# Kernel tuning notes

Measured on AMD Instinct MI355X. Metric: run time of the kernel, lower is better.

Reference implementation:

```python
import jax, jax.numpy as jnp
import numpy as np

N, H, D = 500000, 64, 32  # agents, action_decoder_hidden_dim, distance_embedding_dim


def setup_inputs() -> dict:
    key = jax.random.key(0)
    ks = jax.random.split(key, 8)
    return {
        "action_hidden_state": jax.random.normal(ks[0], (N, H), jnp.float32),
        "goal_hidden_state": jax.random.normal(ks[1], (H,), jnp.float32),
        "goal": jax.random.normal(ks[2], (N, 2), jnp.float32),
        "position": jax.random.normal(ks[3], (N, 2), jnp.float32),
        "W_emb": jax.random.normal(ks[4], (D, 2), jnp.float32) * 0.1,
        "b_emb": jax.random.normal(ks[5], (D,), jnp.float32) * 0.1,
        "W_fc": jax.random.normal(ks[6], (H, 2 * D + 2 * H), jnp.float32) * 0.05,
        "b_fc": jax.random.normal(ks[7], (H,), jnp.float32) * 0.05,
        "idx": 0,
    }


def _distances(a1, a2, g1, g2):
    # a1, g1: (2,); a2, g2: (n, 2). Faithful vectorization of cal_distance,
    # including its algebraic quirks (dn first term is 0; cross_g uses g1[0] twice;
    # n2 mixes a1[1]-a2[0]).
    dn = -(a1[1] - a2[:, 1]) * (g1[0] - g2[:, 0])
    cross_a = a1[0] * a2[:, 1] - a1[1] * a2[:, 0]
    cross_g = g1[0] * g2[:, 1] - g1[0] * g2[:, 0]
    n1 = cross_a * (g1[0] - g2[:, 0]) - (a1[0] - a2[:, 0]) * cross_g
    n2 = cross_a * (g1[1] - g2[:, 1]) - (a1[1] - a2[:, 0]) * cross_g
    d1_base = jnp.linalg.norm(a1 - g1)                 # scalar
    d2_base = jnp.linalg.norm(a2 - g2, axis=-1)        # (n,)
    safe_dn = jnp.where(dn != 0, dn, 1.0)
    p1 = n1 / safe_dn
    p2 = n2 / safe_dn
    cond = (dn != 0) & ((a1[0] - p1) * (p1 - g1[0]) > 0)
    d1_int = jnp.sqrt((a1[0] - p1) ** 2 + (a1[1] - p2) ** 2)
    d2_int = jnp.sqrt((a2[:, 0] - p1) ** 2 + (a2[:, 1] - p2) ** 2)
    return jnp.where(cond, d1_int, d1_base), jnp.where(cond, d2_int, d2_base)


def reference(action_hidden_state, goal_hidden_state, goal, position, W_emb, b_emb, W_fc, b_fc, idx):
    h = action_hidden_state                      # (n, H)
    n, Hd = h.shape
    p_idx = position[idx]                        # (2,)
    d1, d2 = _distances(p_idx, goal, p_idx, position)   # (n,), (n,)
    # embedding(d) with scalar d broadcast to [d, d]: d*(W[:,0]+W[:,1]) + b
    w_sum = W_emb[:, 0] + W_emb[:, 1]            # (D,)
    d1e = d1[:, None] * w_sum[None, :] + b_emb   # (n, D)
    d2e = d2[:, None] * w_sum[None, :] + b_emb   # (n, D)
    h_idx_row = jnp.broadcast_to(h[idx], (n, Hd))
    fc_in = jnp.concatenate([h_idx_row, h, d1e, d2e], axis=1)  # (n, 2H+2D)
    new_h = jax.nn.sigmoid(fc_in @ W_fc.T + b_fc)              # (n, H)
    keep = (jnp.arange(n) == idx)[:, None]       # row idx is skipped in the loop
    h_out = jnp.where(keep, h, new_h)
    # goal update (uses original h[idx], unchanged by the loop)
    dg = jnp.linalg.norm(p_idx - goal[idx])
    dge = dg * w_sum + b_emb                     # (D,)
    fc_in_g = jnp.concatenate([h[idx], goal_hidden_state, dge, dge], axis=0)
    goal_out = jax.nn.sigmoid(W_fc @ fc_in_g + b_fc)
    return h_out, goal_out
```

## Files before the change

### kernel.cpp

```cpp
#include <hip/hip_runtime.h>
#include <math.h>


#define AH 64
#define AD 32

typedef __attribute__((ext_vector_type(8))) short bf16x8;
typedef __attribute__((ext_vector_type(4))) float f32x4;
typedef __attribute__((ext_vector_type(2))) float f32x2;

__device__ __forceinline__ float sigmoid_fast(float x) {
    return 1.0f / (1.0f + __expf(-x));
}

__device__ __forceinline__ short f2bf(float f) {
    union { float f; unsigned u; } v; v.f = f;
    unsigned r = v.u + 0x7fffu + ((v.u >> 16) & 1u);
    return (short)(r >> 16);
}

__global__ __launch_bounds__(256, 4) void ig_fused(
    const float* __restrict__ h,
    const float* __restrict__ ghs,
    const float* __restrict__ goal,
    const float* __restrict__ pos,
    const float* __restrict__ W_emb,
    const float* __restrict__ b_emb,
    const float* __restrict__ W_fc,
    const float* __restrict__ b_fc,
    const int*   __restrict__ idx_p,
    float* __restrict__ out,
    int N, int n_tiles, int total_waves)
{
    __shared__ bf16x8 wlds[8][64];
    __shared__ __align__(16) float cw[128];

    const int tid  = threadIdx.x;
    const int w    = tid >> 6;
    const int lane = tid & 63;
    const int m15  = lane & 15;
    const int q    = lane >> 4;
    const int idx  = idx_p[0];

    if (w == 0) {
        const int l = lane;
        const float* wrow = W_fc + l * 192;
        const f32x4* w4  = (const f32x4*)wrow;
        const f32x4* wg4 = (const f32x4*)(wrow + AH);
        const f32x4* h4  = (const f32x4*)(h + (size_t)idx * AH);
        const f32x4* g4  = (const f32x4*)ghs;
        float c = b_fc[l], g = b_fc[l];
        #pragma unroll
        for (int m = 0; m < 16; ++m) {
            const f32x4 hv = h4[m], wv = w4[m];
            const float d = hv[0]*wv[0] + hv[1]*wv[1] + hv[2]*wv[2] + hv[3]*wv[3];
            c += d; g += d;
            const f32x4 gv = g4[m], wv2 = wg4[m];
            g += gv[0]*wv2[0] + gv[1]*wv2[1] + gv[2]*wv2[2] + gv[3]*wv2[3];
        }
        const float px = pos[(size_t)idx*2+0], py = pos[(size_t)idx*2+1];
        const float gx = goal[(size_t)idx*2+0], gy = goal[(size_t)idx*2+1];
        const float dgx = px - gx, dgy = py - gy;
        const float dg = sqrtf(dgx*dgx + dgy*dgy);
        const float* wd1 = wrow + 128;
        const float* wd2 = wrow + 160;
        float wd = 0.f;
        #pragma unroll
        for (int k = 0; k < AD; ++k) {
            const float wsum = W_emb[2*k] + W_emb[2*k+1];
            const float be   = b_emb[k];
            const float w12  = wd1[k] + wd2[k];
            c  += be * w12;
            wd += wsum * wd2[k];
            g  += (dg * wsum + be) * w12;
        }
        cw[l]      = c;
        cw[64 + l] = wd;
        if (blockIdx.x == 0) out[(size_t)N * AH + l] = sigmoid_fast(g);
    } else {
        for (int f = w - 1; f < 8; f += 3) {
            const int mg = f >> 1, c = f & 1;
            const float* src = W_fc + (size_t)(mg*16 + m15) * 192 + AH + c*32 + q*8;
            const f32x4 s0 = *(const f32x4*)(src);
            const f32x4 s1 = *(const f32x4*)(src + 4);
            bf16x8 b;
            #pragma unroll
            for (int j = 0; j < 4; ++j) { b[j] = f2bf(s0[j]); b[4+j] = f2bf(s1[j]); }
            wlds[f][lane] = b;
        }
    }
    __syncthreads();

    const int wid = blockIdx.x * 4 + w;

    int t = wid;
    f32x4 b0 = {}, b1 = {}, b2 = {}, b3 = {};
    f32x2 gv = {}, pv = {};
    if (t < n_tiles) {
        const int n0 = t * 16 + m15;
        const float* hr = h + (size_t)n0 * AH;
        b0 = *(const f32x4*)(hr + q*8);
        b1 = *(const f32x4*)(hr + q*8 + 4);
        b2 = *(const f32x4*)(hr + 32 + q*8);
        b3 = *(const f32x4*)(hr + 32 + q*8 + 4);
        gv = *(const f32x2*)(goal + 2*(size_t)n0);
        pv = *(const f32x2*)(pos  + 2*(size_t)n0);
    }

    while (t < n_tiles) {
        const int tn = t + total_waves;
        const int tload = (tn < n_tiles) ? tn : t;
        const int nl = tload * 16 + m15;
        const float* hrn = h + (size_t)nl * AH;
        const f32x4 nb0 = *(const f32x4*)(hrn + q*8);
        const f32x4 nb1 = *(const f32x4*)(hrn + q*8 + 4);
        const f32x4 nb2 = *(const f32x4*)(hrn + 32 + q*8);
        const f32x4 nb3 = *(const f32x4*)(hrn + 32 + q*8 + 4);
        const f32x2 ngv = *(const f32x2*)(goal + 2*(size_t)nl);
        const f32x2 npv = *(const f32x2*)(pos  + 2*(size_t)nl);

        const int agent = t * 16 + m15;
        const float dx = gv[0] - pv[0], dy = gv[1] - pv[1];
        const float d2v = sqrtf(dx*dx + dy*dy);

        bf16x8 bf0, bf1;
        #pragma unroll
        for (int j = 0; j < 4; ++j) {
            bf0[j] = f2bf(b0[j]); bf0[4+j] = f2bf(b1[j]);
            bf1[j] = f2bf(b2[j]); bf1[4+j] = f2bf(b3[j]);
        }

        const size_t rb = (size_t)agent * AH;
        #pragma unroll
        for (int mg = 0; mg < 4; ++mg) {
            const f32x4 c4 = *(const f32x4*)&cw[mg*16 + q*4];
            const f32x4 d4 = *(const f32x4*)&cw[64 + mg*16 + q*4];
            f32x4 acc;
            #pragma unroll
            for (int r = 0; r < 4; ++r) acc[r] = c4[r] + d2v * d4[r];
            acc = __builtin_amdgcn_mfma_f32_16x16x32_bf16(wlds[mg*2+0][lane], bf0, acc, 0, 0, 0);
            acc = __builtin_amdgcn_mfma_f32_16x16x32_bf16(wlds[mg*2+1][lane], bf1, acc, 0, 0, 0);

            f32x4 vv;
            #pragma unroll
            for (int r = 0; r < 4; ++r) vv[r] = sigmoid_fast(acc[r]);
            if (agent == idx) vv = *(const f32x4*)(h + rb + mg*16 + q*4);
            __builtin_nontemporal_store(vv, (f32x4*)(out + rb + mg*16 + q*4));
        }

        t = tn;
        b0 = nb0; b1 = nb1; b2 = nb2; b3 = nb3;
        gv = ngv; pv = npv;
    }
}

extern "C" void kernel_launch(void* const* d_in, const int* in_sizes, int n_in,
                              void* d_out, int out_size, void* d_ws, size_t ws_size,
                              hipStream_t stream) {
    const float* h     = (const float*)d_in[0];
    const float* ghs   = (const float*)d_in[1];
    const float* goal  = (const float*)d_in[2];
    const float* pos   = (const float*)d_in[3];
    const float* W_emb = (const float*)d_in[4];
    const float* b_emb = (const float*)d_in[5];
    const float* W_fc  = (const float*)d_in[6];
    const float* b_fc  = (const float*)d_in[7];
    const int*   idx_p = (const int*)d_in[8];

    const int N = in_sizes[0] / AH;
    float* out = (float*)d_out;

    const int n_tiles = N / 16;
    const int blocks = 1280;
    const int total_waves = blocks * 4;
    ig_fused<<<blocks, 256, 0, stream>>>(h, ghs, goal, pos, W_emb, b_emb, W_fc, b_fc,
                                         idx_p, out, N, n_tiles, total_waves);
}
```

Before: 267.2 us.

## Split per-block weight prep into a one-block precompute kernel via workspace

Moves the constant-vector and bf16 weight-fragment computation, previously redone by every block, into a separate single-block kernel that writes the results to workspace. The main kernel then only copies the precomputed values into LDS before its tile loop. The change also swaps the sigmoid divide for a hardware reciprocal, replaces nontemporal stores with regular stores, and drops the grid from 1280 to 1024 blocks. The cost is a second kernel launch and a serial dependency between the two kernels.

```diff
diff --git a/kernel.cpp b/kernel.cpp
--- a/kernel.cpp
+++ b/kernel.cpp
@@ -10,7 +10,7 @@
 typedef __attribute__((ext_vector_type(2))) float f32x2;
 
 __device__ __forceinline__ float sigmoid_fast(float x) {
-    return 1.0f / (1.0f + __expf(-x));
+    return __builtin_amdgcn_rcpf(1.0f + __expf(-x));
 }
 
 __device__ __forceinline__ short f2bf(float f) {
@@ -19,7 +19,7 @@
     return (short)(r >> 16);
 }
 
-__global__ __launch_bounds__(256, 4) void ig_fused(
+__global__ void ig_precompute(
     const float* __restrict__ h,
     const float* __restrict__ ghs,
     const float* __restrict__ goal,
@@ -29,8 +29,70 @@
     const float* __restrict__ W_fc,
     const float* __restrict__ b_fc,
     const int*   __restrict__ idx_p,
+    float* __restrict__ out_goal,
+    float* __restrict__ ws)
+{
+    const int l = threadIdx.x;
+    if (l >= 64) return;
+    const int idx = idx_p[0];
+    const int m15 = l & 15, q = l >> 4;
+
+    const float* wrow = W_fc + l * 192;
+    const f32x4* w4  = (const f32x4*)wrow;
+    const f32x4* wg4 = (const f32x4*)(wrow + AH);
+    const f32x4* h4  = (const f32x4*)(h + (size_t)idx * AH);
+    const f32x4* g4  = (const f32x4*)ghs;
+    float c = b_fc[l], g = b_fc[l];
+    #pragma unroll
+    for (int m = 0; m < 16; ++m) {
+        const f32x4 hv = h4[m], wv = w4[m];
+        const float d = hv[0]*wv[0] + hv[1]*wv[1] + hv[2]*wv[2] + hv[3]*wv[3];
+        c += d; g += d;
+        const f32x4 gv = g4[m], wv2 = wg4[m];
+        g += gv[0]*wv2[0] + gv[1]*wv2[1] + gv[2]*wv2[2] + gv[3]*wv2[3];
+    }
+    const float px = pos[(size_t)idx*2+0], py = pos[(size_t)idx*2+1];
+    const float gx = goal[(size_t)idx*2+0], gy = goal[(size_t)idx*2+1];
+    const float dgx = px - gx, dgy = py - gy;
+    const float dg = sqrtf(dgx*dgx + dgy*dgy);
+    const float* wd1 = wrow + 128;
+    const float* wd2 = wrow + 160;
+    float wd = 0.f;
+    #pragma unroll
+    for (int k = 0; k < AD; ++k) {
+        const float wsum = W_emb[2*k] + W_emb[2*k+1];
+        const float be   = b_emb[k];
+        const float w12  = wd1[k] + wd2[k];
+        c  += be * w12;
+        wd += wsum * wd2[k];
+        g  += (dg * wsum + be) * w12;
+    }
+    ws[l]      = c;
+    ws[64 + l] = wd;
+    out_goal[l] = sigmoid_fast(g);
+
+    bf16x8* wf = (bf16x8*)(ws + 128);
+    #pragma unroll
+    for (int f = 0; f < 8; ++f) {
+        const int mg = f >> 1, cc = f & 1;
+        const float* src = W_fc + (size_t)(mg*16 + m15) * 192 + AH + cc*32 + q*8;
+        const f32x4 s0 = *(const f32x4*)(src);
+        const f32x4 s1 = *(const f32x4*)(src + 4);
+        bf16x8 b;
+        #pragma unroll
+        for (int j = 0; j < 4; ++j) { b[j] = f2bf(s0[j]); b[4+j] = f2bf(s1[j]); }
+        wf[f * 64 + l] = b;
+    }
+}
+
+__global__ __launch_bounds__(256, 4) void ig_main(
+    const float* __restrict__ h,
+    const float* __restrict__ goal,
+    const float* __restrict__ pos,
+    const float* __restrict__ ws,
+    const int*   __restrict__ idx_p,
     float* __restrict__ out,
-    int N, int n_tiles, int total_waves)
+    int n_tiles, int total_waves)
 {
     __shared__ bf16x8 wlds[8][64];
     __shared__ __align__(16) float cw[128];
@@ -42,57 +104,16 @@
     const int q    = lane >> 4;
     const int idx  = idx_p[0];
 
-    if (w == 0) {
-        const int l = lane;
-        const float* wrow = W_fc + l * 192;
-        const f32x4* w4  = (const f32x4*)wrow;
-        const f32x4* wg4 = (const f32x4*)(wrow + AH);
-        const f32x4* h4  = (const f32x4*)(h + (size_t)idx * AH);
-        const f32x4* g4  = (const f32x4*)ghs;
-        float c = b_fc[l], g = b_fc[l];
-        #pragma unroll
-        for (int m = 0; m < 16; ++m) {
-            const f32x4 hv = h4[m], wv = w4[m];
-            const float d = hv[0]*wv[0] + hv[1]*wv[1] + hv[2]*wv[2] + hv[3]*wv[3];
-            c += d; g += d;
-            const f32x4 gv = g4[m], wv2 = wg4[m];
-            g += gv[0]*wv2[0] + gv[1]*wv2[1] + gv[2]*wv2[2] + gv[3]*wv2[3];
-        }
-        const float px = pos[(size_t)idx*2+0], py = pos[(size_t)idx*2+1];
-        const float gx = goal[(size_t)idx*2+0], gy = goal[(size_t)idx*2+1];
-        const float dgx = px - gx, dgy = py - gy;
-        const float dg = sqrtf(dgx*dgx + dgy*dgy);
-        const float* wd1 = wrow + 128;
-        const float* wd2 = wrow + 160;
-        float wd = 0.f;
-        #pragma unroll
-        for (int k = 0; k < AD; ++k) {
-            const float wsum = W_emb[2*k] + W_emb[2*k+1];
-            const float be   = b_emb[k];
-            const float w12  = wd1[k] + wd2[k];
-            c  += be * w12;
-            wd += wsum * wd2[k];
-            g  += (dg * wsum + be) * w12;
-        }
-        cw[l]      = c;
-        cw[64 + l] = wd;
-        if (blockIdx.x == 0) out[(size_t)N * AH + l] = sigmoid_fast(g);
-    } else {
-        for (int f = w - 1; f < 8; f += 3) {
-            const int mg = f >> 1, c = f & 1;
-            const float* src = W_fc + (size_t)(mg*16 + m15) * 192 + AH + c*32 + q*8;
-            const f32x4 s0 = *(const f32x4*)(src);
-            const f32x4 s1 = *(const f32x4*)(src + 4);
-            bf16x8 b;
-            #pragma unroll
-            for (int j = 0; j < 4; ++j) { b[j] = f2bf(s0[j]); b[4+j] = f2bf(s1[j]); }
-            wlds[f][lane] = b;
-        }
+    if (tid < 128) cw[tid] = ws[tid];
+    {
+        const f32x4* src = (const f32x4*)(ws + 128);
+        f32x4* dst = (f32x4*)wlds;
+        dst[tid]       = src[tid];
+        dst[tid + 256] = src[tid + 256];
     }
     __syncthreads();
 
     const int wid = blockIdx.x * 4 + w;
-
     int t = wid;
     f32x4 b0 = {}, b1 = {}, b2 = {}, b3 = {};
     f32x2 gv = {}, pv = {};
@@ -145,7 +166,7 @@
             #pragma unroll
             for (int r = 0; r < 4; ++r) vv[r] = sigmoid_fast(acc[r]);
             if (agent == idx) vv = *(const f32x4*)(h + rb + mg*16 + q*4);
-            __builtin_nontemporal_store(vv, (f32x4*)(out + rb + mg*16 + q*4));
+            *(f32x4*)(out + rb + mg*16 + q*4) = vv;
         }
 
         t = tn;
@@ -168,11 +189,16 @@
     const int*   idx_p = (const int*)d_in[8];
 
     const int N = in_sizes[0] / AH;
-    float* out = (float*)d_out;
+    float* out      = (float*)d_out;
+    float* out_goal = out + (size_t)N * AH;
+    float* ws       = (float*)d_ws;
+
+    ig_precompute<<<1, 64, 0, stream>>>(h, ghs, goal, pos, W_emb, b_emb, W_fc, b_fc,
+                                        idx_p, out_goal, ws);
 
     const int n_tiles = N / 16;
-    const int blocks = 1280;
+    const int blocks = 1024;
     const int total_waves = blocks * 4;
-    ig_fused<<<blocks, 256, 0, stream>>>(h, ghs, goal, pos, W_emb, b_emb, W_fc, b_fc,
-                                         idx_p, out, N, n_tiles, total_waves);
-}
+    ig_main<<<blocks, 256, 0, stream>>>(h, goal, pos, ws, idx_p, out,
+                                        n_tiles, total_waves);
+}
```

After: 256.5 us. -4.0%, faster.
